# Optimization experiments

Hardware: AMD Instinct MI355X
Metric: run time of the kernel (lower is better)

The kernel has to match this reference:

```python
import jax, jax.numpy as jnp
import numpy as np


def setup_inputs() -> dict:
    key = jax.random.key(0)
    k1, k2, k3 = jax.random.split(key, 3)
    B, D, C = 16384, 512, 1000
    features = jax.random.normal(k1, (B, D), dtype=jnp.float32)
    labels = jax.random.randint(k2, (B,), 0, C, dtype=jnp.int64)
    center = jax.random.normal(k3, (D, C), dtype=jnp.float32)  # stacked class centers [d, C]
    return {"features": features, "labels": labels, "center": center}


def reference(features, labels, center):
    # F.normalize(center, p=2, dim=0): unit-norm each class-center column
    eps = 1e-12
    norm = jnp.maximum(jnp.linalg.norm(center, axis=0, keepdims=True), eps)
    c = center / norm                                  # [d, C]
    logits = features @ c                              # [B, C] (replaces per-sample loop)
    log_probs = jax.nn.log_softmax(logits, axis=-1)    # -log(exp(z_y)/sum exp(z))
    nll = -jnp.take_along_axis(log_probs, labels[:, None].astype(jnp.int32), axis=1)[:, 0]
    return jnp.mean(nll)
```

## Files before the change

kernel.cpp:

```cpp
#include <hip/hip_runtime.h>
#include <math.h>

namespace {

constexpr int kB = 16384;
constexpr int kD = 512;
constexpr int kC = 1000;
constexpr float kScale = 64.f;
constexpr float kSinv  = 1.f / 64.f;

typedef __attribute__((ext_vector_type(4))) float f4v;
typedef long long i64b;
union BU { uint4 v; i64b d[2]; };

__device__ inline unsigned int pk4(float a, float b, float c, float d) {
  int r = __builtin_amdgcn_cvt_pk_fp8_f32(a, b, 0, false);
  r = __builtin_amdgcn_cvt_pk_fp8_f32(c, d, r, true);
  return (unsigned int)r;
}

__global__ __launch_bounds__(256)
void k_prep(const float* __restrict__ center, unsigned char* __restrict__ pb,
            float* __restrict__ out) {
  if (blockIdx.x == 0 && threadIdx.x == 0) out[0] = 0.f;
  __shared__ float Ct[kD][16];
  __shared__ float P[16][16];
  __shared__ float inv[16];
  const int t = threadIdx.x, ct = blockIdx.x;
  const int col = t & 15, dg = t >> 4;
  const int cc = ct * 16 + col;
  float s = 0.f;
#pragma unroll 8
  for (int j = 0; j < 32; ++j) {
    int d = dg * 32 + j;
    float v = (cc < kC) ? center[(size_t)d * kC + cc] : 0.f;
    Ct[d][col] = v;
    s = fmaf(v, v, s);
  }
  P[dg][col] = s;
  __syncthreads();
  if (t < 16) {
    float tot = 0.f;
#pragma unroll
    for (int j = 0; j < 16; ++j) tot += P[j][t];
    inv[t] = rsqrtf(fmaxf(tot, 1e-24f)) * kScale;
  }
  __syncthreads();
#pragma unroll
  for (int pi = 0; pi < 4; ++pi) {
    int p = t * 4 + pi;
    int ks = p >> 6, lane = p & 63;
    int cl = lane & 15, d0 = ks * 32 + ((lane >> 4) << 3);
    float iv = inv[cl];
    unsigned int lo = pk4(Ct[d0 + 0][cl] * iv, Ct[d0 + 1][cl] * iv,
                          Ct[d0 + 2][cl] * iv, Ct[d0 + 3][cl] * iv);
    unsigned int hi = pk4(Ct[d0 + 4][cl] * iv, Ct[d0 + 5][cl] * iv,
                          Ct[d0 + 6][cl] * iv, Ct[d0 + 7][cl] * iv);
    *(uint2*)(pb + (size_t)ct * 8192 + (ks >> 1) * 1024 + lane * 16 + (ks & 1) * 8) =
        make_uint2(lo, hi);
  }
}

__global__ __launch_bounds__(256, 3)
void k_main(const float* __restrict__ features,
            const int* __restrict__ labels,
            const unsigned char* __restrict__ pb,
            float* __restrict__ out) {
  __shared__ __align__(16) unsigned char Ab[32 * kD];
  float* Sf = (float*)Ab;
  const int t = threadIdx.x;
  const int w = t >> 6, lane = t & 63;
  const int b0r = blockIdx.x * 32;

#pragma unroll
  for (int i = 0; i < 8; ++i) {
    int ci = i * 256 + t;
    int row = ci >> 6, kc = ci & 63;
    const float* src = features + (size_t)(b0r + row) * kD + kc * 8;
    float4 f0 = *(const float4*)src;
    float4 f1 = *(const float4*)(src + 4);
    unsigned int lo = pk4(f0.x, f0.y, f0.z, f0.w);
    unsigned int hi = pk4(f1.x, f1.y, f1.z, f1.w);
    *(uint2*)(Ab + row * 512 + ((kc * 8) ^ ((row & 7) << 3))) = make_uint2(lo, hi);
  }
  __syncthreads();

  i64b a8[2][16];
#pragma unroll
  for (int rt = 0; rt < 2; ++rt) {
    const int row = rt * 16 + (lane & 15);
    const int rb = row * 512, swz = (row & 7) << 3;
#pragma unroll
    for (int ks = 0; ks < 16; ++ks) {
      const int kc = ks * 4 + (lane >> 4);
      a8[rt][ks] = *(const i64b*)(Ab + rb + ((kc * 8) ^ swz));
    }
  }
#pragma unroll
  for (int rt = 0; rt < 2; ++rt)
#pragma unroll
    for (int ks = 0; ks < 16; ++ks)
      asm volatile("" : "+v"(a8[rt][ks]));

  float l[8], zl[8];
  int lab[8];
#pragma unroll
  for (int s = 0; s < 8; ++s) {
    l[s] = 0.f; zl[s] = 0.f;
    lab[s] = labels[b0r + (s >> 2) * 16 + ((lane >> 4) << 2) + (s & 3)];
  }

  const unsigned char* pbw = pb + (size_t)(w * 16) * 8192 + lane * 16;
  uint4 br[8];
#pragma unroll
  for (int p = 0; p < 6; ++p) br[p] = *(const uint4*)(pbw + p * 1024);

#pragma unroll 1
  for (int i = 0; i < 16; ++i) {
    const unsigned char* pcur = pbw + (size_t)i * 8192;
    const int ct = w * 16 + i;
    const int cls = ct * 16 + (lane & 15);
    const bool valid = cls < kC;

    f4v acc[2][2] = {{{0.f,0.f,0.f,0.f},{0.f,0.f,0.f,0.f}},
                     {{0.f,0.f,0.f,0.f},{0.f,0.f,0.f,0.f}}};
#pragma unroll
    for (int p = 0; p < 8; ++p) {
      {
        const int pp = p + 6;
        br[pp & 7] = *(const uint4*)(pcur + (pp >> 3) * 8192 + (pp & 7) * 1024);
      }
      BU b; b.v = br[p];
      __builtin_amdgcn_s_setprio(1);
      acc[0][0] = __builtin_amdgcn_mfma_f32_16x16x32_fp8_fp8(a8[0][2*p],   b.d[0], acc[0][0], 0, 0, 0);
      acc[1][0] = __builtin_amdgcn_mfma_f32_16x16x32_fp8_fp8(a8[1][2*p],   b.d[0], acc[1][0], 0, 0, 0);
      acc[0][1] = __builtin_amdgcn_mfma_f32_16x16x32_fp8_fp8(a8[0][2*p+1], b.d[1], acc[0][1], 0, 0, 0);
      acc[1][1] = __builtin_amdgcn_mfma_f32_16x16x32_fp8_fp8(a8[1][2*p+1], b.d[1], acc[1][1], 0, 0, 0);
      __builtin_amdgcn_s_setprio(0);
    }

#pragma unroll
    for (int rt = 0; rt < 2; ++rt) {
#pragma unroll
      for (int r = 0; r < 4; ++r) {
        const int s = rt * 4 + r;
        float lg = valid ? (acc[rt][0][r] + acc[rt][1][r]) : -1e30f;
        zl[s] = (cls == lab[s]) ? lg : zl[s];
        l[s] += __expf(lg * kSinv);
      }
    }
  }

  __syncthreads();

#pragma unroll
  for (int s = 0; s < 8; ++s) {
    float L = l[s];
    L += __shfl_xor(L, 1, 64);
    L += __shfl_xor(L, 2, 64);
    L += __shfl_xor(L, 4, 64);
    L += __shfl_xor(L, 8, 64);
    float Z = zl[s];
    Z += __shfl_xor(Z, 1, 64);
    Z += __shfl_xor(Z, 2, 64);
    Z += __shfl_xor(Z, 4, 64);
    Z += __shfl_xor(Z, 8, 64);
    if ((lane & 15) == 0) {
      const int row = (s >> 2) * 16 + ((lane >> 4) << 2) + (s & 3);
      Sf[(row * 4 + w) * 2 + 0] = L;
      Sf[(row * 4 + w) * 2 + 1] = Z;
    }
  }
  __syncthreads();

  if (t < 64) {
    float nll = 0.f;
    if (t < 32) {
      float L = 0.f, Z = 0.f;
#pragma unroll
      for (int j = 0; j < 4; ++j) {
        L += Sf[(t * 4 + j) * 2 + 0];
        Z += Sf[(t * 4 + j) * 2 + 1];
      }
      nll = logf(L) - Z * kSinv;
    }
    nll += __shfl_xor(nll, 1, 64);
    nll += __shfl_xor(nll, 2, 64);
    nll += __shfl_xor(nll, 4, 64);
    nll += __shfl_xor(nll, 8, 64);
    nll += __shfl_xor(nll, 16, 64);
    nll += __shfl_xor(nll, 32, 64);
    if (t == 0) atomicAdd(out, nll * (1.0f / (float)kB));
  }
}

}

extern "C" void kernel_launch(void* const* d_in, const int* in_sizes, int n_in,
                              void* d_out, int out_size, void* d_ws, size_t ws_size,
                              hipStream_t stream) {
  const float* features = (const float*)d_in[0];
  const int* labels     = (const int*)d_in[1];
  const float* center   = (const float*)d_in[2];
  float* out = (float*)d_out;

  unsigned char* pb = (unsigned char*)d_ws;

  k_prep<<<65, 256, 0, stream>>>(center, pb, out);
  k_main<<<kB / 32, 256, 0, stream>>>(features, labels, pb, out);
}
```

Baseline: 39.68 us.

## Double rows per block and compute label logit exactly in fp32 via gather

The main kernel now handles 64 rows per block with 512 threads, so each warp covers half as many class tiles but four row tiles, and each fetched B fragment feeds more MFMAs. The label logit is no longer picked out of the fp8 MFMA accumulators. The prep kernel now writes a normalized fp32 copy of the centers, and the main kernel gathers each label's center row and dots it with the fp32 features while loading them. The softmax exponent is folded into a single exp2 of an fma, with a bias that masks padded classes. The cost is extra global reads for the gathered center rows, more VGPRs for the A fragments, and a change in occupancy.

```diff
diff --git a/kernel.cpp b/kernel.cpp
--- a/kernel.cpp
+++ b/kernel.cpp
@@ -7,7 +7,7 @@
 constexpr int kD = 512;
 constexpr int kC = 1000;
 constexpr float kScale = 64.f;
-constexpr float kSinv  = 1.f / 64.f;
+constexpr float kC2 = (1.f / 64.f) * 1.44269504f;
 
 typedef __attribute__((ext_vector_type(4))) float f4v;
 typedef long long i64b;
@@ -21,7 +21,7 @@
 
 __global__ __launch_bounds__(256)
 void k_prep(const float* __restrict__ center, unsigned char* __restrict__ pb,
-            float* __restrict__ out) {
+            float* __restrict__ cn, float* __restrict__ out) {
   if (blockIdx.x == 0 && threadIdx.x == 0) out[0] = 0.f;
   __shared__ float Ct[kD][16];
   __shared__ float P[16][16];
@@ -43,15 +43,21 @@
     float tot = 0.f;
 #pragma unroll
     for (int j = 0; j < 16; ++j) tot += P[j][t];
-    inv[t] = rsqrtf(fmaxf(tot, 1e-24f)) * kScale;
-  }
-  __syncthreads();
+    inv[t] = rsqrtf(fmaxf(tot, 1e-24f));
+  }
+  __syncthreads();
+  if (ct < 64) {
+    float iv = inv[col];
+#pragma unroll
+    for (int j = 0; j < 32; ++j)
+      cn[(size_t)cc * kD + dg * 32 + j] = Ct[dg * 32 + j][col] * iv;
+  }
 #pragma unroll
   for (int pi = 0; pi < 4; ++pi) {
     int p = t * 4 + pi;
     int ks = p >> 6, lane = p & 63;
     int cl = lane & 15, d0 = ks * 32 + ((lane >> 4) << 3);
-    float iv = inv[cl];
+    float iv = inv[cl] * kScale;
     unsigned int lo = pk4(Ct[d0 + 0][cl] * iv, Ct[d0 + 1][cl] * iv,
                           Ct[d0 + 2][cl] * iv, Ct[d0 + 3][cl] * iv);
     unsigned int hi = pk4(Ct[d0 + 4][cl] * iv, Ct[d0 + 5][cl] * iv,
@@ -61,33 +67,48 @@
   }
 }
 
-__global__ __launch_bounds__(256, 3)
+__global__ __launch_bounds__(512, 2)
 void k_main(const float* __restrict__ features,
             const int* __restrict__ labels,
             const unsigned char* __restrict__ pb,
+            const float* __restrict__ cn,
             float* __restrict__ out) {
-  __shared__ __align__(16) unsigned char Ab[32 * kD];
-  float* Sf = (float*)Ab;
+  __shared__ __align__(16) unsigned char Ab[64 * kD];
+  __shared__ float Sl[64][8];
+  __shared__ float Zw[8];
   const int t = threadIdx.x;
   const int w = t >> 6, lane = t & 63;
-  const int b0r = blockIdx.x * 32;
-
+  const int b0r = blockIdx.x * 64;
+
+  float zp = 0.f;
 #pragma unroll
   for (int i = 0; i < 8; ++i) {
-    int ci = i * 256 + t;
+    int ci = i * 512 + t;
     int row = ci >> 6, kc = ci & 63;
     const float* src = features + (size_t)(b0r + row) * kD + kc * 8;
     float4 f0 = *(const float4*)src;
     float4 f1 = *(const float4*)(src + 4);
+    const float* cnp = cn + (size_t)labels[b0r + row] * kD + kc * 8;
+    float4 c0 = *(const float4*)cnp;
+    float4 c1 = *(const float4*)(cnp + 4);
+    zp += f0.x * c0.x + f0.y * c0.y + f0.z * c0.z + f0.w * c0.w +
+          f1.x * c1.x + f1.y * c1.y + f1.z * c1.z + f1.w * c1.w;
     unsigned int lo = pk4(f0.x, f0.y, f0.z, f0.w);
     unsigned int hi = pk4(f1.x, f1.y, f1.z, f1.w);
     *(uint2*)(Ab + row * 512 + ((kc * 8) ^ ((row & 7) << 3))) = make_uint2(lo, hi);
   }
-  __syncthreads();
-
-  i64b a8[2][16];
-#pragma unroll
-  for (int rt = 0; rt < 2; ++rt) {
+  zp += __shfl_xor(zp, 1, 64);
+  zp += __shfl_xor(zp, 2, 64);
+  zp += __shfl_xor(zp, 4, 64);
+  zp += __shfl_xor(zp, 8, 64);
+  zp += __shfl_xor(zp, 16, 64);
+  zp += __shfl_xor(zp, 32, 64);
+  if (lane == 0) Zw[w] = zp;
+  __syncthreads();
+
+  i64b a8[4][16];
+#pragma unroll
+  for (int rt = 0; rt < 4; ++rt) {
     const int row = rt * 16 + (lane & 15);
     const int rb = row * 512, swz = (row & 7) << 3;
 #pragma unroll
@@ -97,33 +118,28 @@
     }
   }
 #pragma unroll
-  for (int rt = 0; rt < 2; ++rt)
+  for (int rt = 0; rt < 4; ++rt)
 #pragma unroll
     for (int ks = 0; ks < 16; ++ks)
       asm volatile("" : "+v"(a8[rt][ks]));
 
-  float l[8], zl[8];
-  int lab[8];
-#pragma unroll
-  for (int s = 0; s < 8; ++s) {
-    l[s] = 0.f; zl[s] = 0.f;
-    lab[s] = labels[b0r + (s >> 2) * 16 + ((lane >> 4) << 2) + (s & 3)];
-  }
-
-  const unsigned char* pbw = pb + (size_t)(w * 16) * 8192 + lane * 16;
+  float l[16];
+#pragma unroll
+  for (int s = 0; s < 16; ++s) l[s] = 0.f;
+
+  const unsigned char* pbw = pb + (size_t)(w * 8) * 8192 + lane * 16;
   uint4 br[8];
 #pragma unroll
   for (int p = 0; p < 6; ++p) br[p] = *(const uint4*)(pbw + p * 1024);
 
 #pragma unroll 1
-  for (int i = 0; i < 16; ++i) {
+  for (int i = 0; i < 8; ++i) {
     const unsigned char* pcur = pbw + (size_t)i * 8192;
-    const int ct = w * 16 + i;
-    const int cls = ct * 16 + (lane & 15);
-    const bool valid = cls < kC;
-
-    f4v acc[2][2] = {{{0.f,0.f,0.f,0.f},{0.f,0.f,0.f,0.f}},
-                     {{0.f,0.f,0.f,0.f},{0.f,0.f,0.f,0.f}}};
+    const int cls = (w * 8 + i) * 16 + (lane & 15);
+    const float bias = (cls < kC) ? 0.f : -1e30f;
+
+    f4v acc[4][2] = {{{0,0,0,0},{0,0,0,0}}, {{0,0,0,0},{0,0,0,0}},
+                     {{0,0,0,0},{0,0,0,0}}, {{0,0,0,0},{0,0,0,0}}};
 #pragma unroll
     for (int p = 0; p < 8; ++p) {
       {
@@ -132,65 +148,56 @@
       }
       BU b; b.v = br[p];
       __builtin_amdgcn_s_setprio(1);
-      acc[0][0] = __builtin_amdgcn_mfma_f32_16x16x32_fp8_fp8(a8[0][2*p],   b.d[0], acc[0][0], 0, 0, 0);
-      acc[1][0] = __builtin_amdgcn_mfma_f32_16x16x32_fp8_fp8(a8[1][2*p],   b.d[0], acc[1][0], 0, 0, 0);
-      acc[0][1] = __builtin_amdgcn_mfma_f32_16x16x32_fp8_fp8(a8[0][2*p+1], b.d[1], acc[0][1], 0, 0, 0);
-      acc[1][1] = __builtin_amdgcn_mfma_f32_16x16x32_fp8_fp8(a8[1][2*p+1], b.d[1], acc[1][1], 0, 0, 0);
+#pragma unroll
+      for (int rt = 0; rt < 4; ++rt) {
+        acc[rt][0] = __builtin_amdgcn_mfma_f32_16x16x32_fp8_fp8(
+            a8[rt][2 * p], b.d[0], acc[rt][0], 0, 0, 0);
+        acc[rt][1] = __builtin_amdgcn_mfma_f32_16x16x32_fp8_fp8(
+            a8[rt][2 * p + 1], b.d[1], acc[rt][1], 0, 0, 0);
+      }
       __builtin_amdgcn_s_setprio(0);
     }
 
 #pragma unroll
-    for (int rt = 0; rt < 2; ++rt) {
+    for (int rt = 0; rt < 4; ++rt)
 #pragma unroll
       for (int r = 0; r < 4; ++r) {
-        const int s = rt * 4 + r;
-        float lg = valid ? (acc[rt][0][r] + acc[rt][1][r]) : -1e30f;
-        zl[s] = (cls == lab[s]) ? lg : zl[s];
-        l[s] += __expf(lg * kSinv);
+        float lg = acc[rt][0][r] + acc[rt][1][r];
+        l[rt * 4 + r] += exp2f(fmaf(lg, kC2, bias));
       }
-    }
-  }
-
-  __syncthreads();
-
-#pragma unroll
-  for (int s = 0; s < 8; ++s) {
+  }
+
+#pragma unroll
+  for (int s = 0; s < 16; ++s) {
     float L = l[s];
     L += __shfl_xor(L, 1, 64);
     L += __shfl_xor(L, 2, 64);
     L += __shfl_xor(L, 4, 64);
     L += __shfl_xor(L, 8, 64);
-    float Z = zl[s];
-    Z += __shfl_xor(Z, 1, 64);
-    Z += __shfl_xor(Z, 2, 64);
-    Z += __shfl_xor(Z, 4, 64);
-    Z += __shfl_xor(Z, 8, 64);
     if ((lane & 15) == 0) {
       const int row = (s >> 2) * 16 + ((lane >> 4) << 2) + (s & 3);
-      Sf[(row * 4 + w) * 2 + 0] = L;
-      Sf[(row * 4 + w) * 2 + 1] = Z;
+      Sl[row][w] = L;
     }
   }
   __syncthreads();
 
   if (t < 64) {
-    float nll = 0.f;
-    if (t < 32) {
-      float L = 0.f, Z = 0.f;
-#pragma unroll
-      for (int j = 0; j < 4; ++j) {
-        L += Sf[(t * 4 + j) * 2 + 0];
-        Z += Sf[(t * 4 + j) * 2 + 1];
-      }
-      nll = logf(L) - Z * kSinv;
-    }
+    float L = 0.f;
+#pragma unroll
+    for (int j = 0; j < 8; ++j) L += Sl[t][j];
+    float nll = __logf(L);
     nll += __shfl_xor(nll, 1, 64);
     nll += __shfl_xor(nll, 2, 64);
     nll += __shfl_xor(nll, 4, 64);
     nll += __shfl_xor(nll, 8, 64);
     nll += __shfl_xor(nll, 16, 64);
     nll += __shfl_xor(nll, 32, 64);
-    if (t == 0) atomicAdd(out, nll * (1.0f / (float)kB));
+    if (t == 0) {
+      float Z = 0.f;
+#pragma unroll
+      for (int j = 0; j < 8; ++j) Z += Zw[j];
+      atomicAdd(out, (nll - Z) * (1.0f / (float)kB));
+    }
   }
 }
 
@@ -205,7 +212,8 @@
   float* out = (float*)d_out;
 
   unsigned char* pb = (unsigned char*)d_ws;
-
-  k_prep<<<65, 256, 0, stream>>>(center, pb, out);
-  k_main<<<kB / 32, 256, 0, stream>>>(features, labels, pb, out);
-}
+  float* cn = (float*)((char*)d_ws + 65 * 8192);
+
+  k_prep<<<65, 256, 0, stream>>>(center, pb, cn, out);
+  k_main<<<kB / 64, 512, 0, stream>>>(features, labels, pb, cn, out);
+}
```

Result: slower. 44.80 us (+12.9%).

## Double-buffer center tiles with inline-asm async loads and manual waitcnt

Applied to the files above, without the earlier changes.

The main loop now keeps two full 8-register buffers of packed fp8 center data and processes two class tiles per iteration. Loads go through inline-asm global_load_dwordx4, with an explicit s_waitcnt vmcnt(8), so the next tile's fetch overlaps the current tile's MFMAs. The occupancy hint drops from 3 to 2 blocks per CU to make room for the extra registers. The exponential becomes exp2f with the log2e factor folded into the scale, and the prep kernel loses its extra block that nothing read. The hand-managed waitcnt relies on the compiler not reordering around the asm loads, which is a correctness risk.

```diff
diff --git a/kernel.cpp b/kernel.cpp
--- a/kernel.cpp
+++ b/kernel.cpp
@@ -8,6 +8,7 @@
 constexpr int kC = 1000;
 constexpr float kScale = 64.f;
 constexpr float kSinv  = 1.f / 64.f;
+constexpr float kC2    = kSinv * 1.44269504f;
 
 typedef __attribute__((ext_vector_type(4))) float f4v;
 typedef long long i64b;
@@ -17,6 +18,10 @@
   int r = __builtin_amdgcn_cvt_pk_fp8_f32(a, b, 0, false);
   r = __builtin_amdgcn_cvt_pk_fp8_f32(c, d, r, true);
   return (unsigned int)r;
+}
+
+__device__ inline void ld_async(uint4& dst, const void* addr) {
+  asm volatile("global_load_dwordx4 %0, %1, off" : "=v"(dst) : "v"(addr));
 }
 
 __global__ __launch_bounds__(256)
@@ -61,7 +66,7 @@
   }
 }
 
-__global__ __launch_bounds__(256, 3)
+__global__ __launch_bounds__(256, 2)
 void k_main(const float* __restrict__ features,
             const int* __restrict__ labels,
             const unsigned char* __restrict__ pb,
@@ -109,47 +114,56 @@
     l[s] = 0.f; zl[s] = 0.f;
     lab[s] = labels[b0r + (s >> 2) * 16 + ((lane >> 4) << 2) + (s & 3)];
   }
+#pragma unroll
+  for (int s = 0; s < 8; ++s) asm volatile("" : "+v"(lab[s]));
 
   const unsigned char* pbw = pb + (size_t)(w * 16) * 8192 + lane * 16;
-  uint4 br[8];
-#pragma unroll
-  for (int p = 0; p < 6; ++p) br[p] = *(const uint4*)(pbw + p * 1024);
+  uint4 bA[8], bB[8];
+
+#pragma unroll
+  for (int p = 0; p < 8; ++p) ld_async(bA[p], pbw + p * 1024);
+#pragma unroll
+  for (int p = 0; p < 8; ++p) ld_async(bB[p], pbw + 8192 + p * 1024);
+
+#define TILE_BODY(buf, tidx, nidx)                                            \
+  {                                                                           \
+    const int ct = w * 16 + (tidx);                                           \
+    const int cls = ct * 16 + (lane & 15);                                    \
+    const bool valid = cls < kC;                                              \
+    const unsigned char* pnx = pbw + (size_t)((nidx) & 15) * 8192;            \
+    asm volatile("s_waitcnt vmcnt(8)" ::: "memory");                          \
+    __builtin_amdgcn_sched_barrier(0);                                        \
+    f4v acc[2][2] = {{{0.f,0.f,0.f,0.f},{0.f,0.f,0.f,0.f}},                   \
+                     {{0.f,0.f,0.f,0.f},{0.f,0.f,0.f,0.f}}};                  \
+    _Pragma("unroll") for (int p = 0; p < 8; ++p) {                           \
+      BU b; b.v = buf[p];                                                     \
+      __builtin_amdgcn_s_setprio(1);                                          \
+      acc[0][0] = __builtin_amdgcn_mfma_f32_16x16x32_fp8_fp8(                 \
+          a8[0][2 * p], b.d[0], acc[0][0], 0, 0, 0);                          \
+      acc[1][0] = __builtin_amdgcn_mfma_f32_16x16x32_fp8_fp8(                 \
+          a8[1][2 * p], b.d[0], acc[1][0], 0, 0, 0);                          \
+      acc[0][1] = __builtin_amdgcn_mfma_f32_16x16x32_fp8_fp8(                 \
+          a8[0][2 * p + 1], b.d[1], acc[0][1], 0, 0, 0);                      \
+      acc[1][1] = __builtin_amdgcn_mfma_f32_16x16x32_fp8_fp8(                 \
+          a8[1][2 * p + 1], b.d[1], acc[1][1], 0, 0, 0);                      \
+      __builtin_amdgcn_s_setprio(0);                                          \
+      ld_async(buf[p], pnx + p * 1024);     \
+    }                                                                         \
+    _Pragma("unroll") for (int rt = 0; rt < 2; ++rt)                          \
+    _Pragma("unroll") for (int r = 0; r < 4; ++r) {                           \
+      const int s = rt * 4 + r;                                               \
+      float lg = valid ? (acc[rt][0][r] + acc[rt][1][r]) : -1e30f;            \
+      zl[s] = (cls == lab[s]) ? lg : zl[s];                                   \
+      l[s] += exp2f(lg * kC2);                                                \
+    }                                                                         \
+  }
 
 #pragma unroll 1
-  for (int i = 0; i < 16; ++i) {
-    const unsigned char* pcur = pbw + (size_t)i * 8192;
-    const int ct = w * 16 + i;
-    const int cls = ct * 16 + (lane & 15);
-    const bool valid = cls < kC;
-
-    f4v acc[2][2] = {{{0.f,0.f,0.f,0.f},{0.f,0.f,0.f,0.f}},
-                     {{0.f,0.f,0.f,0.f},{0.f,0.f,0.f,0.f}}};
-#pragma unroll
-    for (int p = 0; p < 8; ++p) {
-      {
-        const int pp = p + 6;
-        br[pp & 7] = *(const uint4*)(pcur + (pp >> 3) * 8192 + (pp & 7) * 1024);
-      }
-      BU b; b.v = br[p];
-      __builtin_amdgcn_s_setprio(1);
-      acc[0][0] = __builtin_amdgcn_mfma_f32_16x16x32_fp8_fp8(a8[0][2*p],   b.d[0], acc[0][0], 0, 0, 0);
-      acc[1][0] = __builtin_amdgcn_mfma_f32_16x16x32_fp8_fp8(a8[1][2*p],   b.d[0], acc[1][0], 0, 0, 0);
-      acc[0][1] = __builtin_amdgcn_mfma_f32_16x16x32_fp8_fp8(a8[0][2*p+1], b.d[1], acc[0][1], 0, 0, 0);
-      acc[1][1] = __builtin_amdgcn_mfma_f32_16x16x32_fp8_fp8(a8[1][2*p+1], b.d[1], acc[1][1], 0, 0, 0);
-      __builtin_amdgcn_s_setprio(0);
-    }
-
-#pragma unroll
-    for (int rt = 0; rt < 2; ++rt) {
-#pragma unroll
-      for (int r = 0; r < 4; ++r) {
-        const int s = rt * 4 + r;
-        float lg = valid ? (acc[rt][0][r] + acc[rt][1][r]) : -1e30f;
-        zl[s] = (cls == lab[s]) ? lg : zl[s];
-        l[s] += __expf(lg * kSinv);
-      }
-    }
-  }
+  for (int ii = 0; ii < 8; ++ii) {
+    TILE_BODY(bA, 2 * ii,     2 * ii + 2);
+    TILE_BODY(bB, 2 * ii + 1, 2 * ii + 3);
+  }
+#undef TILE_BODY
 
   __syncthreads();
 
@@ -206,6 +220,6 @@
 
   unsigned char* pb = (unsigned char*)d_ws;
 
-  k_prep<<<65, 256, 0, stream>>>(center, pb, out);
+  k_prep<<<64, 256, 0, stream>>>(center, pb, out);
   k_main<<<kB / 32, 256, 0, stream>>>(features, labels, pb, out);
 }
```

Result: slower. 40.61 us (+2.3%).

## Split class range across two blocks per row tile with separate finalize kernel

Applied to the files above, without the earlier changes.

Each 32-row tile is now handled by two blocks, each covering half of the class tiles. This doubles the grid to raise occupancy and parallelism on the GPU. Partial sum-exp and label-logit values are accumulated atomically into per-row workspace buffers, and a new finalize kernel applies log and the mean. The cost is converting features to fp8 twice per row tile, extra atomics, and a third kernel launch. The exp is also switched to exp2f with a folded log2(e) constant.

```diff
diff --git a/kernel.cpp b/kernel.cpp
--- a/kernel.cpp
+++ b/kernel.cpp
@@ -8,6 +8,7 @@
 constexpr int kC = 1000;
 constexpr float kScale = 64.f;
 constexpr float kSinv  = 1.f / 64.f;
+constexpr float kC2    = kSinv * 1.44269504f;
 
 typedef __attribute__((ext_vector_type(4))) float f4v;
 typedef long long i64b;
@@ -21,8 +22,13 @@
 
 __global__ __launch_bounds__(256)
 void k_prep(const float* __restrict__ center, unsigned char* __restrict__ pb,
+            float* __restrict__ Lp, float* __restrict__ Zp,
             float* __restrict__ out) {
   if (blockIdx.x == 0 && threadIdx.x == 0) out[0] = 0.f;
+  if (blockIdx.x < 64) {
+    Lp[blockIdx.x * 256 + threadIdx.x] = 0.f;
+    Zp[blockIdx.x * 256 + threadIdx.x] = 0.f;
+  }
   __shared__ float Ct[kD][16];
   __shared__ float P[16][16];
   __shared__ float inv[16];
@@ -65,12 +71,13 @@
 void k_main(const float* __restrict__ features,
             const int* __restrict__ labels,
             const unsigned char* __restrict__ pb,
-            float* __restrict__ out) {
+            float* __restrict__ Lp, float* __restrict__ Zp) {
   __shared__ __align__(16) unsigned char Ab[32 * kD];
   float* Sf = (float*)Ab;
   const int t = threadIdx.x;
   const int w = t >> 6, lane = t & 63;
-  const int b0r = blockIdx.x * 32;
+  const int rb = blockIdx.x >> 1, h = blockIdx.x & 1;
+  const int b0r = rb * 32;
 
 #pragma unroll
   for (int i = 0; i < 8; ++i) {
@@ -89,11 +96,11 @@
 #pragma unroll
   for (int rt = 0; rt < 2; ++rt) {
     const int row = rt * 16 + (lane & 15);
-    const int rb = row * 512, swz = (row & 7) << 3;
+    const int rbyte = row * 512, swz = (row & 7) << 3;
 #pragma unroll
     for (int ks = 0; ks < 16; ++ks) {
       const int kc = ks * 4 + (lane >> 4);
-      a8[rt][ks] = *(const i64b*)(Ab + rb + ((kc * 8) ^ swz));
+      a8[rt][ks] = *(const i64b*)(Ab + rbyte + ((kc * 8) ^ swz));
     }
   }
 #pragma unroll
@@ -110,15 +117,16 @@
     lab[s] = labels[b0r + (s >> 2) * 16 + ((lane >> 4) << 2) + (s & 3)];
   }
 
-  const unsigned char* pbw = pb + (size_t)(w * 16) * 8192 + lane * 16;
+  const int tbase = h * 32 + w * 8;
+  const unsigned char* pbw = pb + (size_t)tbase * 8192 + lane * 16;
   uint4 br[8];
 #pragma unroll
   for (int p = 0; p < 6; ++p) br[p] = *(const uint4*)(pbw + p * 1024);
 
 #pragma unroll 1
-  for (int i = 0; i < 16; ++i) {
+  for (int i = 0; i < 8; ++i) {
     const unsigned char* pcur = pbw + (size_t)i * 8192;
-    const int ct = w * 16 + i;
+    const int ct = tbase + i;
     const int cls = ct * 16 + (lane & 15);
     const bool valid = cls < kC;
 
@@ -146,7 +154,7 @@
         const int s = rt * 4 + r;
         float lg = valid ? (acc[rt][0][r] + acc[rt][1][r]) : -1e30f;
         zl[s] = (cls == lab[s]) ? lg : zl[s];
-        l[s] += __expf(lg * kSinv);
+        l[s] += exp2f(lg * kC2);
       }
     }
   }
@@ -173,25 +181,35 @@
   }
   __syncthreads();
 
-  if (t < 64) {
-    float nll = 0.f;
-    if (t < 32) {
-      float L = 0.f, Z = 0.f;
-#pragma unroll
-      for (int j = 0; j < 4; ++j) {
-        L += Sf[(t * 4 + j) * 2 + 0];
-        Z += Sf[(t * 4 + j) * 2 + 1];
-      }
-      nll = logf(L) - Z * kSinv;
-    }
-    nll += __shfl_xor(nll, 1, 64);
-    nll += __shfl_xor(nll, 2, 64);
-    nll += __shfl_xor(nll, 4, 64);
-    nll += __shfl_xor(nll, 8, 64);
-    nll += __shfl_xor(nll, 16, 64);
-    nll += __shfl_xor(nll, 32, 64);
-    if (t == 0) atomicAdd(out, nll * (1.0f / (float)kB));
-  }
+  if (t < 32) {
+    float L = 0.f, Z = 0.f;
+#pragma unroll
+    for (int j = 0; j < 4; ++j) {
+      L += Sf[(t * 4 + j) * 2 + 0];
+      Z += Sf[(t * 4 + j) * 2 + 1];
+    }
+    atomicAdd(&Lp[b0r + t], L);
+    atomicAdd(&Zp[b0r + t], Z);
+  }
+}
+
+__global__ __launch_bounds__(256)
+void k_fin(const float* __restrict__ Lp, const float* __restrict__ Zp,
+           float* __restrict__ out) {
+  __shared__ float W[4];
+  const int t = threadIdx.x;
+  const int row = blockIdx.x * 256 + t;
+  float nll = __logf(Lp[row]) - Zp[row] * kSinv;
+  nll += __shfl_xor(nll, 1, 64);
+  nll += __shfl_xor(nll, 2, 64);
+  nll += __shfl_xor(nll, 4, 64);
+  nll += __shfl_xor(nll, 8, 64);
+  nll += __shfl_xor(nll, 16, 64);
+  nll += __shfl_xor(nll, 32, 64);
+  if ((t & 63) == 0) W[t >> 6] = nll;
+  __syncthreads();
+  if (t == 0)
+    atomicAdd(out, (W[0] + W[1] + W[2] + W[3]) * (1.0f / (float)kB));
 }
 
 }
@@ -205,7 +223,10 @@
   float* out = (float*)d_out;
 
   unsigned char* pb = (unsigned char*)d_ws;
-
-  k_prep<<<65, 256, 0, stream>>>(center, pb, out);
-  k_main<<<kB / 32, 256, 0, stream>>>(features, labels, pb, out);
-}
+  float* Lp = (float*)((char*)d_ws + 65 * 8192);
+  float* Zp = Lp + kB;
+
+  k_prep<<<65, 256, 0, stream>>>(center, pb, Lp, Zp, out);
+  k_main<<<kB / 32 * 2, 256, 0, stream>>>(features, labels, pb, Lp, Zp);
+  k_fin <<<kB / 256, 256, 0, stream>>>(Lp, Zp, out);
+}
```

Result: slower. 42.83 us (+8.0%).
